# Kernel optimization log

Hardware: AMD Instinct MI355X
Metric: run time of the kernel (lower is better)

The kernel has to match this reference:

```python
import jax, jax.numpy as jnp
import numpy as np

BETA = 0.95
THR = 1.0
NUM_STEPS = 25
NUM_IN, NUM_HID, NUM_OUT = 9, 100, 2
BATCH = 65536


def _heaviside(x):
    return (x > 0).astype(x.dtype)


def setup_inputs() -> dict:
    key = jax.random.key(0)
    ks = jax.random.split(key, 5)
    x = jax.random.normal(ks[0], (BATCH, NUM_IN), dtype=jnp.float32)
    # nn.Linear default init: U(-1/sqrt(fan_in), 1/sqrt(fan_in))
    b1lim = 1.0 / np.sqrt(NUM_IN)
    b2lim = 1.0 / np.sqrt(NUM_HID)
    W1 = jax.random.uniform(ks[1], (NUM_HID, NUM_IN), jnp.float32, -b1lim, b1lim)
    b1 = jax.random.uniform(ks[2], (NUM_HID,), jnp.float32, -b1lim, b1lim)
    W2 = jax.random.uniform(ks[3], (NUM_OUT, NUM_HID), jnp.float32, -b2lim, b2lim)
    b2 = jax.random.uniform(ks[4], (NUM_OUT,), jnp.float32, -b2lim, b2lim)
    return {"x": x, "W1": W1, "b1": b1, "W2": W2, "b2": b2}


def reference(x, W1, b1, W2, b2):
    # cur1 = fc1(x) is identical every step (x is static) -> hoist out of loop
    cur1 = x @ W1.T + b1                     # [B, 100]
    mem1 = jnp.zeros((x.shape[0], NUM_HID), x.dtype)
    mem2 = jnp.zeros((x.shape[0], NUM_OUT), x.dtype)

    def step(carry, _):
        mem1, mem2 = carry
        # snntorch Leaky, reset_mechanism='subtract': reset from PREVIOUS mem
        reset1 = _heaviside(mem1 - THR)
        mem1 = BETA * mem1 + cur1 - reset1 * THR
        spk1 = _heaviside(mem1 - THR)        # [B, 100]
        cur2 = spk1 @ W2.T + b2              # [B, 2]
        reset2 = _heaviside(mem2 - THR)
        mem2 = BETA * mem2 + cur2 - reset2 * THR
        return (mem1, mem2), mem2

    (_, _), mem2_rec = jax.lax.scan(step, (mem1, mem2), None, length=NUM_STEPS)
    return mem2_rec                          # [25, B, 2]
```

## Files before the change

### kernel.cpp

```cpp
#include <hip/hip_runtime.h>

#define BATCH  65536
#define NIN    9
#define NHID   100
#define TSTEPS 25
#define CHUNK  5

typedef float v2f __attribute__((ext_vector_type(2)));

__global__ __launch_bounds__(256) void snn_kernel(
    const float* __restrict__ x,  const float* __restrict__ W1,
    const float* __restrict__ b1, const float* __restrict__ W2,
    const float* __restrict__ b2, float* __restrict__ out)
{
    __shared__ float sx[64 * NIN];
    __shared__ v2f   sacc[2][4][CHUNK][64];

    const int tid  = threadIdx.x;
    const int lane = tid & 63;
    const int wq   = __builtin_amdgcn_readfirstlane(tid >> 6);
    const int b0   = blockIdx.x * 64;

    for (int i = tid; i < 64 * NIN; i += 256) sx[i] = x[(size_t)b0 * NIN + i];
    __syncthreads();

    double xv[NIN];
#pragma unroll
    for (int i = 0; i < NIN; ++i) xv[i] = (double)sx[lane * NIN + i];

    float a0[TSTEPS], a1[TSTEPS];
#pragma unroll
    for (int t = 0; t < TSTEPS; ++t) { a0[t] = 0.f; a1[t] = 0.f; }

    const int h0 = wq * 25;
#pragma unroll 1
    for (int j = 0; j < 25; ++j) {
        const int h = h0 + j;
        double c = 0.0;
#pragma unroll
        for (int i = 0; i < NIN; ++i)
            c += (double)W1[h * NIN + i] * xv[i];
        c += (double)b1[h];
        double c1 = c - 1.0;
        float w0 = W2[h], w1 = W2[NHID + h];

        double m = 0.0;
        bool s = false;
#pragma unroll
        for (int t = 0; t < TSTEPS; ++t) {
            m = 0.95 * m + (s ? c1 : c);
            s = (m > 1.0);
            float d = s ? 1.f : 0.f;
            asm("v_fmac_f32 %0, %1, %2" : "+v"(a0[t]) : "v"(d), "v"(w0));
            asm("v_fmac_f32 %0, %1, %2" : "+v"(a1[t]) : "v"(d), "v"(w1));
        }
    }

    double m20 = 0.0, m21 = 0.0;
    double bb0 = (double)b2[0], bb1 = (double)b2[1];

#pragma unroll
    for (int k = 0; k < TSTEPS / CHUNK; ++k) {
#pragma unroll
        for (int u = 0; u < CHUNK; ++u)
            sacc[k & 1][wq][u][lane] = (v2f){a0[k * CHUNK + u], a1[k * CHUNK + u]};
        __syncthreads();
        if (wq == 0) {
#pragma unroll
            for (int u = 0; u < CHUNK; ++u) {
                const int t = k * CHUNK + u;
                v2f q0 = sacc[k & 1][0][u][lane];
                v2f q1 = sacc[k & 1][1][u][lane];
                v2f q2 = sacc[k & 1][2][u][lane];
                v2f q3 = sacc[k & 1][3][u][lane];
                v2f sum = (q0 + q1) + (q2 + q3);
                double r0 = (m20 > 1.0) ? 1.0 : 0.0;
                double r1 = (m21 > 1.0) ? 1.0 : 0.0;
                m20 = 0.95 * m20 + ((double)sum[0] + bb0) - r0;
                m21 = 0.95 * m21 + ((double)sum[1] + bb1) - r1;
                *(float2*)(out + ((size_t)t * BATCH + b0 + lane) * 2) =
                    make_float2((float)m20, (float)m21);
            }
        }
    }
}

extern "C" void kernel_launch(void* const* d_in, const int* in_sizes, int n_in,
                              void* d_out, int out_size, void* d_ws, size_t ws_size,
                              hipStream_t stream) {
    const float* x  = (const float*)d_in[0];
    const float* W1 = (const float*)d_in[1];
    const float* b1 = (const float*)d_in[2];
    const float* W2 = (const float*)d_in[3];
    const float* b2 = (const float*)d_in[4];
    float* out = (float*)d_out;

    dim3 grid(BATCH / 64), block(256);
    hipLaunchKernelGGL(snn_kernel, grid, block, 0, stream, x, W1, b1, W2, b2, out);
}
```

Baseline: 99.23 us.

## Run membrane recurrence in fp32 with fp64 fallback near threshold

The per-hidden-neuron membrane recurrence and input projection switch from double to single precision, and the program tracks the minimum distance of the membrane to the threshold. If any lane comes within a small epsilon of the threshold, a wavefront-wide fallback reruns that neuron in double precision alongside fp32 and corrects the accumulated output wherever the spike decisions differ. The goal is to avoid slow fp64 arithmetic in the hot loop while keeping the spike decisions of the double-precision path. The cost is extra register pressure, a divergent branch, and a fallback rerun whenever any lane nears the threshold.

```diff
diff --git a/kernel.cpp b/kernel.cpp
--- a/kernel.cpp
+++ b/kernel.cpp
@@ -5,6 +5,7 @@
 #define NHID   100
 #define TSTEPS 25
 #define CHUNK  5
+#define EPS    5e-5f
 
 typedef float v2f __attribute__((ext_vector_type(2)));
 
@@ -24,35 +25,61 @@
     for (int i = tid; i < 64 * NIN; i += 256) sx[i] = x[(size_t)b0 * NIN + i];
     __syncthreads();
 
-    double xv[NIN];
+    float xv[NIN];
 #pragma unroll
-    for (int i = 0; i < NIN; ++i) xv[i] = (double)sx[lane * NIN + i];
+    for (int i = 0; i < NIN; ++i) xv[i] = sx[lane * NIN + i];
 
-    float a0[TSTEPS], a1[TSTEPS];
+    v2f acc[TSTEPS];
 #pragma unroll
-    for (int t = 0; t < TSTEPS; ++t) { a0[t] = 0.f; a1[t] = 0.f; }
+    for (int t = 0; t < TSTEPS; ++t) acc[t] = (v2f){0.f, 0.f};
 
     const int h0 = wq * 25;
 #pragma unroll 1
     for (int j = 0; j < 25; ++j) {
         const int h = h0 + j;
-        double c = 0.0;
+        float c32 = 0.f;
 #pragma unroll
-        for (int i = 0; i < NIN; ++i)
-            c += (double)W1[h * NIN + i] * xv[i];
-        c += (double)b1[h];
-        double c1 = c - 1.0;
-        float w0 = W2[h], w1 = W2[NHID + h];
+        for (int i = 0; i < NIN; ++i) c32 = fmaf(W1[h * NIN + i], xv[i], c32);
+        c32 += b1[h];
+        const float c1_32 = c32 - 1.0f;
+        const float w0 = W2[h], w1 = W2[NHID + h];
+        const v2f   w  = (v2f){w0, w1};
 
-        double m = 0.0;
-        bool s = false;
+        float m = 0.f, ming = 1e30f;
+        bool  s = false;
 #pragma unroll
         for (int t = 0; t < TSTEPS; ++t) {
-            m = 0.95 * m + (s ? c1 : c);
-            s = (m > 1.0);
+            float cs = s ? c1_32 : c32;
+            m = fmaf(0.95f, m, cs);
+            float g = m - 1.0f;
+            s = (g > 0.0f);
+            ming = fminf(ming, fabsf(g));
             float d = s ? 1.f : 0.f;
-            asm("v_fmac_f32 %0, %1, %2" : "+v"(a0[t]) : "v"(d), "v"(w0));
-            asm("v_fmac_f32 %0, %1, %2" : "+v"(a1[t]) : "v"(d), "v"(w1));
+            acc[t] += (v2f){d, d} * w;
+        }
+
+        if (__any(ming < EPS)) {
+            double c64 = 0.0;
+#pragma unroll
+            for (int i = 0; i < NIN; ++i)
+                c64 += (double)W1[h * NIN + i] * (double)xv[i];
+            c64 += (double)b1[h];
+            const double c1_64 = c64 - 1.0;
+
+            double md = 0.0;  bool sd = false;
+            float  mr = 0.f;  bool sr = false;
+#pragma unroll
+            for (int t = 0; t < TSTEPS; ++t) {
+                float csr = sr ? c1_32 : c32;
+                mr = fmaf(0.95f, mr, csr);
+                sr = ((mr - 1.0f) > 0.0f);
+                md = 0.95 * md + (sd ? c1_64 : c64);
+                sd = (md > 1.0);
+                if (sr != sd) {
+                    float sg = sd ? 1.f : -1.f;
+                    acc[t] += (v2f){sg, sg} * w;
+                }
+            }
         }
     }
 
@@ -63,7 +90,7 @@
     for (int k = 0; k < TSTEPS / CHUNK; ++k) {
 #pragma unroll
         for (int u = 0; u < CHUNK; ++u)
-            sacc[k & 1][wq][u][lane] = (v2f){a0[k * CHUNK + u], a1[k * CHUNK + u]};
+            sacc[k & 1][wq][u][lane] = acc[k * CHUNK + u];
         __syncthreads();
         if (wq == 0) {
 #pragma unroll
```

Result: slower. 102.3 us (+3.1%).
